# Optimization experiments

Measured on AMD Instinct MI355X. Metric: run time of the kernel, lower is better.

Reference implementation:

```python
import jax, jax.numpy as jnp
import numpy as np
from jax import lax

B, T, C, DIN, DOUT = 32, 128, 64, 32, 32  # batch, output_channels(seq), input_channels, input_dim, output_dim


def _init_params(key):
    # Mirror torch init: xOps zeros with identity on min(dout,din) diag; hOps = eye.
    # Add small noise so gradients/behavior are non-degenerate.
    k1, k2 = jax.random.split(key)
    eye_x = jnp.zeros((DOUT, DIN), jnp.float32).at[jnp.arange(min(DOUT, DIN)), jnp.arange(min(DOUT, DIN))].set(1.0)
    xOps = jnp.broadcast_to(eye_x, (4, T, C, DOUT, DIN)) + 0.02 * jax.random.normal(k1, (4, T, C, DOUT, DIN), jnp.float32)
    hOps = jnp.broadcast_to(jnp.eye(DOUT, dtype=jnp.float32), (4, T, C, DOUT, DOUT)) + 0.02 * jax.random.normal(k2, (4, T, C, DOUT, DOUT), jnp.float32)
    return xOps, hOps


def setup_inputs() -> dict:
    key = jax.random.key(0)
    kx, kp = jax.random.split(key)
    x = jax.random.normal(kx, (B, T, C, DIN), jnp.float32)
    xOps, hOps = _init_params(kp)
    return {"x": x, "xOps": xOps, "hOps": hOps}


def reference(x, xOps, hOps):
    # x: [B,T,C,Din]; xOps: [4,T,C,Dout,Din]; hOps: [4,T,C,Dout,Dout]
    b, t, c, _ = x.shape
    dout = hOps.shape[-1]
    h0 = jnp.zeros((b, c, dout), x.dtype)
    c0 = jnp.zeros((b, c, dout), x.dtype)

    def step(carry, inp):
        h, cc = carry
        x_t, xop_t, hop_t = inp  # [B,C,Din], [4,C,Dout,Din], [4,C,Dout,Dout]
        # per-channel (grouped) gate pre-activations, 4 gates at once
        X = jnp.einsum('gcij,bcj->gbci', xop_t, x_t) + jnp.einsum('gcij,bcj->gbci', hop_t, h)
        i = jax.nn.sigmoid(X[0])
        f = jax.nn.sigmoid(X[1])
        g = jnp.tanh(X[2])
        o = jax.nn.sigmoid(X[3])
        c_new = f * cc + i * g
        h_new = o * jnp.tanh(c_new)
        return (h_new, c_new), None

    xs = (jnp.swapaxes(x, 0, 1), jnp.swapaxes(xOps, 0, 1), jnp.swapaxes(hOps, 0, 1))
    (h_fin, _), _ = lax.scan(step, (h0, c0), xs)
    return h_fin  # [B,C,Dout]
```

## Files before the change

kernel.cpp:

```cpp
#include <hip/hip_runtime.h>
#include <stdint.h>

#define T_STEPS 128
#define C_CH    64
#define PIPE    4

using frag_ab = __attribute__((ext_vector_type(8))) short;
using frag_cd = __attribute__((ext_vector_type(4))) float;
typedef __attribute__((ext_vector_type(4))) uint32_t u32x4;

__device__ __forceinline__ uint32_t pack_hi16(uint32_t u0, uint32_t u1) {
  return __builtin_amdgcn_perm(u1, u0, 0x07060302u);
}

__device__ __forceinline__ float fast_sigmoid(float v) {
  return __builtin_amdgcn_rcpf(1.0f + __expf(-v));
}
__device__ __forceinline__ float fast_tanh(float v) {
  return fmaf(2.0f, __builtin_amdgcn_rcpf(1.0f + __expf(-2.0f * v)), -1.0f);
}

__device__ __forceinline__ void async_load16(const float* g, void* l) {
  __builtin_amdgcn_global_load_lds((const __attribute__((address_space(1))) void*)g,
                                   (__attribute__((address_space(3))) void*)l, 16, 0, 0);
}

struct Frag2 { frag_ab hi, lo; };

__device__ __forceinline__ Frag2 split8(float4 a, float4 b) {
  uint32_t u0 = __float_as_uint(a.x), u1 = __float_as_uint(a.y);
  uint32_t u2 = __float_as_uint(a.z), u3 = __float_as_uint(a.w);
  uint32_t u4 = __float_as_uint(b.x), u5 = __float_as_uint(b.y);
  uint32_t u6 = __float_as_uint(b.z), u7 = __float_as_uint(b.w);
  uint32_t r0 = __float_as_uint(a.x - __uint_as_float(u0 & 0xFFFF0000u));
  uint32_t r1 = __float_as_uint(a.y - __uint_as_float(u1 & 0xFFFF0000u));
  uint32_t r2 = __float_as_uint(a.z - __uint_as_float(u2 & 0xFFFF0000u));
  uint32_t r3 = __float_as_uint(a.w - __uint_as_float(u3 & 0xFFFF0000u));
  uint32_t r4 = __float_as_uint(b.x - __uint_as_float(u4 & 0xFFFF0000u));
  uint32_t r5 = __float_as_uint(b.y - __uint_as_float(u5 & 0xFFFF0000u));
  uint32_t r6 = __float_as_uint(b.z - __uint_as_float(u6 & 0xFFFF0000u));
  uint32_t r7 = __float_as_uint(b.w - __uint_as_float(u7 & 0xFFFF0000u));
  union { u32x4 v; frag_ab f; } H, L;
  H.v[0] = pack_hi16(u0, u1); H.v[1] = pack_hi16(u2, u3);
  H.v[2] = pack_hi16(u4, u5); H.v[3] = pack_hi16(u6, u7);
  L.v[0] = pack_hi16(r0, r1); L.v[1] = pack_hi16(r2, r3);
  L.v[2] = pack_hi16(r4, r5); L.v[3] = pack_hi16(r6, r7);
  Frag2 o; o.hi = H.f; o.lo = L.f; return o;
}

__global__ void __launch_bounds__(512)
lstm_kernel(const float* __restrict__ x, const float* __restrict__ xOps,
            const float* __restrict__ hOps, float* __restrict__ out) {
  __shared__ __align__(16) float Afp[PIPE][2][128][32];
  __shared__ __align__(16) float Bx[PIPE][16][32];
  __shared__ __align__(16) float Bh[2][16][32];
  __shared__ __align__(16) float Scr[256];

  const int tid    = threadIdx.x;
  const int c      = blockIdx.x & 63;
  const int q      = blockIdx.x >> 6;
  const int w      = tid >> 6;
  const int lane   = tid & 63;
  const int frag_n = lane & 15;
  const int quad   = lane >> 4;

  int apl[4], arb[4];
  const float* aptr[4];
#pragma unroll
  for (int ii = 0; ii < 4; ++ii) {
    const int idx = w + 8 * ii;
    const int pl  = idx >> 4;
    const int rb  = idx & 15;
    apl[ii] = pl; arb[ii] = rb;
    const int r    = rb * 8 + (lane >> 3);
    const int g    = r >> 5;
    const int i    = r & 31;
    const int f    = ((r >> 5) << 1) | (r & 1);
    const int slot = (lane & 7) ^ f;
    const float* base = pl ? hOps : xOps;
    aptr[ii] = base + ((size_t)g * T_STEPS * C_CH + c) * 1024
                    + (size_t)i * 32 + slot * 4;
  }

  const int xn  = lane >> 3, xsl = lane & 7;
  const float* xsrc = x + (((size_t)(q * 8 + xn) * T_STEPS) * C_CH + c) * 32
                        + ((xsl ^ (xn & 7)) << 2);
  const float* dummy_src = xOps;

  for (int i = tid; i < 2 * 16 * 32; i += 512) ((float*)Bh)[i] = 0.f;
  for (int i = tid; i < PIPE * 16 * 32; i += 512) ((float*)Bx)[i] = 0.f;
  __syncthreads();

#pragma unroll
  for (int s0 = 0; s0 < PIPE - 1; ++s0) {
#pragma unroll
    for (int ii = 0; ii < 4; ++ii) {
      async_load16(aptr[ii], &Afp[s0][apl[ii]][arb[ii] * 8][0]);
      aptr[ii] += (size_t)C_CH * 1024;
    }
    if (w == 7) { async_load16(xsrc, &Bx[s0][0][0]); xsrc += (size_t)C_CH * 32; }
  }

  const int frow = (frag_n & 3) * 32 + 4 * w + (frag_n >> 2);
  const int ff   = ((frow >> 5) << 1) | (frow & 1);
  const int so0  = (((quad << 1) ^ ff) << 2);
  const int so1  = ((((quad << 1) | 1) ^ ff) << 2);
  const int bs0  = (((quad << 1) ^ (frag_n & 7)) << 2);
  const int bs1  = ((((quad << 1) | 1) ^ (frag_n & 7)) << 2);
  const int iq   = 4 * w + quad;
  const int hwi  = ((w ^ (frag_n & 7)) << 2) | quad;

  float c_state = 0.0f;

#pragma unroll 4
  for (int t = 0; t < T_STEPS; ++t) {
    const int cb = t & (PIPE - 1);
    const int hp = t & 1;

    if (w == 7) asm volatile("s_waitcnt vmcnt(10) lgkmcnt(0)" ::: "memory");
    else        asm volatile("s_waitcnt vmcnt(8) lgkmcnt(0)" ::: "memory");
    asm volatile("s_barrier" ::: "memory");

    {
      const int s = t + PIPE - 1;
      if (s < T_STEPS) {
        const int sb = s & (PIPE - 1);
#pragma unroll
        for (int ii = 0; ii < 4; ++ii) {
          async_load16(aptr[ii], &Afp[sb][apl[ii]][arb[ii] * 8][0]);
          aptr[ii] += (size_t)C_CH * 1024;
        }
        if (w == 7) { async_load16(xsrc, &Bx[sb][0][0]); xsrc += (size_t)C_CH * 32; }
      } else {
#pragma unroll
        for (int ii = 0; ii < 4; ++ii) async_load16(dummy_src, &Scr[0]);
        if (w == 7) async_load16(dummy_src, &Scr[0]);
      }
    }

    frag_cd acc = {0.f, 0.f, 0.f, 0.f};
    {
      const float* Ap = &Afp[cb][0][frow][0];
      Frag2 A = split8(*(const float4*)(Ap + so0), *(const float4*)(Ap + so1));
      const float* Bp = &Bx[cb][frag_n][0];
      Frag2 Bf = split8(*(const float4*)(Bp + bs0), *(const float4*)(Bp + bs1));
      acc = __builtin_amdgcn_mfma_f32_16x16x32_bf16(A.hi, Bf.hi, acc, 0, 0, 0);
      acc = __builtin_amdgcn_mfma_f32_16x16x32_bf16(A.hi, Bf.lo, acc, 0, 0, 0);
      acc = __builtin_amdgcn_mfma_f32_16x16x32_bf16(A.lo, Bf.hi, acc, 0, 0, 0);
    }
    {
      const float* Ap = &Afp[cb][1][frow][0];
      Frag2 A = split8(*(const float4*)(Ap + so0), *(const float4*)(Ap + so1));
      const float* Bp = &Bh[hp][frag_n][0];
      Frag2 Bf = split8(*(const float4*)(Bp + bs0), *(const float4*)(Bp + bs1));
      acc = __builtin_amdgcn_mfma_f32_16x16x32_bf16(A.hi, Bf.hi, acc, 0, 0, 0);
      acc = __builtin_amdgcn_mfma_f32_16x16x32_bf16(A.hi, Bf.lo, acc, 0, 0, 0);
      acc = __builtin_amdgcn_mfma_f32_16x16x32_bf16(A.lo, Bf.hi, acc, 0, 0, 0);
    }

    const float ig = fast_sigmoid(acc[0]);
    const float fg = fast_sigmoid(acc[1]);
    const float gg = fast_tanh(acc[2]);
    const float og = fast_sigmoid(acc[3]);
    c_state = fg * c_state + ig * gg;
    const float hval = og * fast_tanh(c_state);

    if (t == T_STEPS - 1) {
      if (frag_n < 8)
        out[((size_t)(q * 8 + frag_n) * C_CH + c) * 32 + iq] = hval;
    } else {
      if (frag_n < 8) Bh[hp ^ 1][frag_n][hwi] = hval;
    }
  }
}

extern "C" void kernel_launch(void* const* d_in, const int* in_sizes, int n_in,
                              void* d_out, int out_size, void* d_ws, size_t ws_size,
                              hipStream_t stream) {
  const float* x    = (const float*)d_in[0];
  const float* xOps = (const float*)d_in[1];
  const float* hOps = (const float*)d_in[2];
  lstm_kernel<<<dim3(256), dim3(512), 0, stream>>>(x, xOps, hOps, (float*)d_out);
}
```

Measured before the change: 335.4 us.

## Load LSTM weights straight into registers and keep h as split bf16 in LDS

Drops the LDS staging of the xOps/hOps/x tiles via async global-to-LDS loads. Each lane now loads its own MFMA fragment from global memory into registers, in a 3-step-deep register ring. The input projection is computed before the per-step barrier, so only the recurrent MFMAs sit on the critical path. The hidden state is stored in LDS pre-split into bf16 hi/lo halves in a padded layout, so readers skip the split work. Launch bounds now request 2 blocks per CU. The trade-offs are more registers, less coalesced per-lane global loads, and unmasked prefetch latency.

```diff
diff --git a/kernel.cpp b/kernel.cpp
--- a/kernel.cpp
+++ b/kernel.cpp
@@ -3,7 +3,7 @@
 
 #define T_STEPS 128
 #define C_CH    64
-#define PIPE    4
+#define HS      40
 
 using frag_ab = __attribute__((ext_vector_type(8))) short;
 using frag_cd = __attribute__((ext_vector_type(4))) float;
@@ -18,11 +18,6 @@
 }
 __device__ __forceinline__ float fast_tanh(float v) {
   return fmaf(2.0f, __builtin_amdgcn_rcpf(1.0f + __expf(-2.0f * v)), -1.0f);
-}
-
-__device__ __forceinline__ void async_load16(const float* g, void* l) {
-  __builtin_amdgcn_global_load_lds((const __attribute__((address_space(1))) void*)g,
-                                   (__attribute__((address_space(3))) void*)l, 16, 0, 0);
 }
 
 struct Frag2 { frag_ab hi, lo; };
@@ -48,13 +43,11 @@
   Frag2 o; o.hi = H.f; o.lo = L.f; return o;
 }
 
-__global__ void __launch_bounds__(512)
+__global__ void __launch_bounds__(512, 2)
 lstm_kernel(const float* __restrict__ x, const float* __restrict__ xOps,
             const float* __restrict__ hOps, float* __restrict__ out) {
-  __shared__ __align__(16) float Afp[PIPE][2][128][32];
-  __shared__ __align__(16) float Bx[PIPE][16][32];
-  __shared__ __align__(16) float Bh[2][16][32];
-  __shared__ __align__(16) float Scr[256];
+  __shared__ short Hhi[2][16][HS];
+  __shared__ short Hlo[2][16][HS];
 
   const int tid    = threadIdx.x;
   const int c      = blockIdx.x & 63;
@@ -64,112 +57,89 @@
   const int frag_n = lane & 15;
   const int quad   = lane >> 4;
 
-  int apl[4], arb[4];
-  const float* aptr[4];
+  const int g  = frag_n & 3;
+  const int iw = 4 * w + (frag_n >> 2);
+  const size_t woff = ((size_t)g * T_STEPS * C_CH + c) * 1024
+                    + (size_t)iw * 32 + quad * 8;
+  const int bcl = (q * 8 + frag_n) & 31;
+  const size_t xoff = ((size_t)bcl * T_STEPS * C_CH + c) * 32 + quad * 8;
+
+  for (int idx = tid; idx < 2 * 16 * HS; idx += 512) {
+    ((short*)Hhi)[idx] = 0; ((short*)Hlo)[idx] = 0;
+  }
+  __syncthreads();
+
+  float4 wv[4][6];
 #pragma unroll
-  for (int ii = 0; ii < 4; ++ii) {
-    const int idx = w + 8 * ii;
-    const int pl  = idx >> 4;
-    const int rb  = idx & 15;
-    apl[ii] = pl; arb[ii] = rb;
-    const int r    = rb * 8 + (lane >> 3);
-    const int g    = r >> 5;
-    const int i    = r & 31;
-    const int f    = ((r >> 5) << 1) | (r & 1);
-    const int slot = (lane & 7) ^ f;
-    const float* base = pl ? hOps : xOps;
-    aptr[ii] = base + ((size_t)g * T_STEPS * C_CH + c) * 1024
-                    + (size_t)i * 32 + slot * 4;
+  for (int s = 0; s < 3; ++s) {
+    const float* pw = xOps + (size_t)s * (C_CH * 1024) + woff;
+    wv[s][0] = ((const float4*)pw)[0];
+    wv[s][1] = ((const float4*)pw)[1];
+    const float* ph = hOps + (size_t)s * (C_CH * 1024) + woff;
+    wv[s][2] = ((const float4*)ph)[0];
+    wv[s][3] = ((const float4*)ph)[1];
+    const float* px = x + (size_t)s * (C_CH * 32) + xoff;
+    wv[s][4] = ((const float4*)px)[0];
+    wv[s][5] = ((const float4*)px)[1];
   }
 
-  const int xn  = lane >> 3, xsl = lane & 7;
-  const float* xsrc = x + (((size_t)(q * 8 + xn) * T_STEPS) * C_CH + c) * 32
-                        + ((xsl ^ (xn & 7)) << 2);
-  const float* dummy_src = xOps;
-
-  for (int i = tid; i < 2 * 16 * 32; i += 512) ((float*)Bh)[i] = 0.f;
-  for (int i = tid; i < PIPE * 16 * 32; i += 512) ((float*)Bx)[i] = 0.f;
-  __syncthreads();
-
-#pragma unroll
-  for (int s0 = 0; s0 < PIPE - 1; ++s0) {
-#pragma unroll
-    for (int ii = 0; ii < 4; ++ii) {
-      async_load16(aptr[ii], &Afp[s0][apl[ii]][arb[ii] * 8][0]);
-      aptr[ii] += (size_t)C_CH * 1024;
-    }
-    if (w == 7) { async_load16(xsrc, &Bx[s0][0][0]); xsrc += (size_t)C_CH * 32; }
-  }
-
-  const int frow = (frag_n & 3) * 32 + 4 * w + (frag_n >> 2);
-  const int ff   = ((frow >> 5) << 1) | (frow & 1);
-  const int so0  = (((quad << 1) ^ ff) << 2);
-  const int so1  = ((((quad << 1) | 1) ^ ff) << 2);
-  const int bs0  = (((quad << 1) ^ (frag_n & 7)) << 2);
-  const int bs1  = ((((quad << 1) | 1) ^ (frag_n & 7)) << 2);
-  const int iq   = 4 * w + quad;
-  const int hwi  = ((w ^ (frag_n & 7)) << 2) | quad;
-
+  const int hrd = quad * 8;
+  const int iq  = 4 * w + quad;
   float c_state = 0.0f;
 
-#pragma unroll 4
-  for (int t = 0; t < T_STEPS; ++t) {
-    const int cb = t & (PIPE - 1);
-    const int hp = t & 1;
+  for (int tb = 0; tb < T_STEPS; tb += 4) {
+#pragma unroll
+    for (int u = 0; u < 4; ++u) {
+      const int t  = tb + u;
+      const int cs = u;
+      const int ps = (u + 3) & 3;
 
-    if (w == 7) asm volatile("s_waitcnt vmcnt(10) lgkmcnt(0)" ::: "memory");
-    else        asm volatile("s_waitcnt vmcnt(8) lgkmcnt(0)" ::: "memory");
-    asm volatile("s_barrier" ::: "memory");
+      Frag2 A0 = split8(wv[cs][0], wv[cs][1]);
+      Frag2 A1 = split8(wv[cs][2], wv[cs][3]);
+      Frag2 BX = split8(wv[cs][4], wv[cs][5]);
+      frag_cd ax = {0.f, 0.f, 0.f, 0.f};
+      ax = __builtin_amdgcn_mfma_f32_16x16x32_bf16(A0.hi, BX.hi, ax, 0, 0, 0);
+      ax = __builtin_amdgcn_mfma_f32_16x16x32_bf16(A0.hi, BX.lo, ax, 0, 0, 0);
+      ax = __builtin_amdgcn_mfma_f32_16x16x32_bf16(A0.lo, BX.hi, ax, 0, 0, 0);
 
-    {
-      const int s = t + PIPE - 1;
-      if (s < T_STEPS) {
-        const int sb = s & (PIPE - 1);
-#pragma unroll
-        for (int ii = 0; ii < 4; ++ii) {
-          async_load16(aptr[ii], &Afp[sb][apl[ii]][arb[ii] * 8][0]);
-          aptr[ii] += (size_t)C_CH * 1024;
-        }
-        if (w == 7) { async_load16(xsrc, &Bx[sb][0][0]); xsrc += (size_t)C_CH * 32; }
-      } else {
-#pragma unroll
-        for (int ii = 0; ii < 4; ++ii) async_load16(dummy_src, &Scr[0]);
-        if (w == 7) async_load16(dummy_src, &Scr[0]);
+      if (t + 3 < T_STEPS) {
+        const float* pw = xOps + (size_t)(t + 3) * (C_CH * 1024) + woff;
+        wv[ps][0] = ((const float4*)pw)[0];
+        wv[ps][1] = ((const float4*)pw)[1];
+        const float* ph = hOps + (size_t)(t + 3) * (C_CH * 1024) + woff;
+        wv[ps][2] = ((const float4*)ph)[0];
+        wv[ps][3] = ((const float4*)ph)[1];
+        const float* px = x + (size_t)(t + 3) * (C_CH * 32) + xoff;
+        wv[ps][4] = ((const float4*)px)[0];
+        wv[ps][5] = ((const float4*)px)[1];
       }
-    }
 
-    frag_cd acc = {0.f, 0.f, 0.f, 0.f};
-    {
-      const float* Ap = &Afp[cb][0][frow][0];
-      Frag2 A = split8(*(const float4*)(Ap + so0), *(const float4*)(Ap + so1));
-      const float* Bp = &Bx[cb][frag_n][0];
-      Frag2 Bf = split8(*(const float4*)(Bp + bs0), *(const float4*)(Bp + bs1));
-      acc = __builtin_amdgcn_mfma_f32_16x16x32_bf16(A.hi, Bf.hi, acc, 0, 0, 0);
-      acc = __builtin_amdgcn_mfma_f32_16x16x32_bf16(A.hi, Bf.lo, acc, 0, 0, 0);
-      acc = __builtin_amdgcn_mfma_f32_16x16x32_bf16(A.lo, Bf.hi, acc, 0, 0, 0);
-    }
-    {
-      const float* Ap = &Afp[cb][1][frow][0];
-      Frag2 A = split8(*(const float4*)(Ap + so0), *(const float4*)(Ap + so1));
-      const float* Bp = &Bh[hp][frag_n][0];
-      Frag2 Bf = split8(*(const float4*)(Bp + bs0), *(const float4*)(Bp + bs1));
-      acc = __builtin_amdgcn_mfma_f32_16x16x32_bf16(A.hi, Bf.hi, acc, 0, 0, 0);
-      acc = __builtin_amdgcn_mfma_f32_16x16x32_bf16(A.hi, Bf.lo, acc, 0, 0, 0);
-      acc = __builtin_amdgcn_mfma_f32_16x16x32_bf16(A.lo, Bf.hi, acc, 0, 0, 0);
-    }
+      asm volatile("s_waitcnt lgkmcnt(0)\n\ts_barrier" ::: "memory");
 
-    const float ig = fast_sigmoid(acc[0]);
-    const float fg = fast_sigmoid(acc[1]);
-    const float gg = fast_tanh(acc[2]);
-    const float og = fast_sigmoid(acc[3]);
-    c_state = fg * c_state + ig * gg;
-    const float hval = og * fast_tanh(c_state);
+      const int p = t & 1;
+      const frag_ab bh = *(const frag_ab*)&Hhi[p][frag_n][hrd];
+      const frag_ab bl = *(const frag_ab*)&Hlo[p][frag_n][hrd];
+      frag_cd ah = {0.f, 0.f, 0.f, 0.f};
+      ah = __builtin_amdgcn_mfma_f32_16x16x32_bf16(A1.hi, bh, ah, 0, 0, 0);
+      ah = __builtin_amdgcn_mfma_f32_16x16x32_bf16(A1.hi, bl, ah, 0, 0, 0);
+      ah = __builtin_amdgcn_mfma_f32_16x16x32_bf16(A1.lo, bh, ah, 0, 0, 0);
 
-    if (t == T_STEPS - 1) {
-      if (frag_n < 8)
-        out[((size_t)(q * 8 + frag_n) * C_CH + c) * 32 + iq] = hval;
-    } else {
-      if (frag_n < 8) Bh[hp ^ 1][frag_n][hwi] = hval;
+      const float ig = fast_sigmoid(ax[0] + ah[0]);
+      const float fg = fast_sigmoid(ax[1] + ah[1]);
+      const float gg = fast_tanh(ax[2] + ah[2]);
+      const float og = fast_sigmoid(ax[3] + ah[3]);
+      c_state = fg * c_state + ig * gg;
+      const float hval = og * fast_tanh(c_state);
+
+      if (t == T_STEPS - 1) {
+        if (frag_n < 8)
+          out[((size_t)(q * 8 + frag_n) * C_CH + c) * 32 + iq] = hval;
+      } else if (frag_n < 8) {
+        const uint32_t uh = __float_as_uint(hval);
+        const float    rh = hval - __uint_as_float(uh & 0xFFFF0000u);
+        Hhi[p ^ 1][frag_n][iq] = (short)(uh >> 16);
+        Hlo[p ^ 1][frag_n][iq] = (short)(__float_as_uint(rh) >> 16);
+      }
     }
   }
 }
```

Measured after the change: 375.4 us. 1.12x slower.
